# Kernel tuning notes

Hardware: AMD Instinct MI355X
Metric: run time of the kernel (lower is better)

Reference implementation:

```python
import jax, jax.numpy as jnp
import numpy as np
import math

B, S, E, A, H, L, V = 2, 2048, 512, 512, 8, 4, 50257
HD = A // H  # 64 per-head dim (attention_size // n_heads)
PAD = 0
EPS = 1e-5

def _sin_pe():
    pos = np.arange(S)[:, None].astype(np.float32)
    div = np.exp(np.arange(0, E, 2).astype(np.float32) * (-math.log(10000.0) / E))
    pe = np.zeros((S, E), dtype=np.float32)
    pe[:, 0::2] = np.sin(pos * div)
    pe[:, 1::2] = np.cos(pos * div)
    return jnp.asarray(pe)

PE = _sin_pe()

def setup_inputs():
    key = jax.random.key(0)
    ks = jax.random.split(key, 20)
    s = 0.02
    emb = jax.random.normal(ks[0], (V, E), jnp.float32) * s
    emb = emb.at[PAD].set(0.0)  # nn.Embedding padding_idx row is zero
    return {
        "input_ids": jax.random.randint(ks[1], (B, S), 0, V, dtype=jnp.int32),
        "attention_mask": jnp.ones((B, S), jnp.int32),
        "emb": emb,
        "Wq": jax.random.normal(ks[2], (L, H, E, HD), jnp.float32) * s,
        "Wk": jax.random.normal(ks[3], (L, H, E, HD), jnp.float32) * s,
        "Wv": jax.random.normal(ks[4], (L, H, E, HD), jnp.float32) * s,
        "Wo": jax.random.normal(ks[5], (L, A, E), jnp.float32) * s,
        "ln1_g": jnp.ones((L, E), jnp.float32),
        "ln1_b": jnp.zeros((L, E), jnp.float32),
        "ln2_g": jnp.ones((L, E), jnp.float32),
        "ln2_b": jnp.zeros((L, E), jnp.float32),
        "ff_w1": jax.random.normal(ks[6], (L, E, 4 * E), jnp.float32) * s,
        "ff_b1": jnp.zeros((L, 4 * E), jnp.float32),
        "ff_w2": jax.random.normal(ks[7], (L, 4 * E, E), jnp.float32) * s,
        "ff_b2": jnp.zeros((L, E), jnp.float32),
        "lnf_g": jnp.ones((E,), jnp.float32),
        "lnf_b": jnp.zeros((E,), jnp.float32),
        "Wout": jax.random.normal(ks[8], (E, V), jnp.float32) * s,
        "bout": jnp.zeros((V,), jnp.float32),
    }

def _ln(x, g, b):
    m = jnp.mean(x, axis=-1, keepdims=True)
    v = jnp.mean((x - m) ** 2, axis=-1, keepdims=True)
    return (x - m) / jnp.sqrt(v + EPS) * g + b

def reference(input_ids, attention_mask, emb, Wq, Wk, Wv, Wo, ln1_g, ln1_b, ln2_g, ln2_b, ff_w1, ff_b1, ff_w2, ff_b2, lnf_g, lnf_b, Wout, bout):
    # mask: padding (attention_mask==0) broadcast over queries, OR causal upper triangle
    pad = (attention_mask == 0)[:, None, :]                  # [B,1,S]
    causal = jnp.triu(jnp.ones((S, S), bool), 1)             # [S,S]
    mask = (pad | causal)[:, None, :, :]                     # [B,1,S,S]
    x = emb[input_ids] + PE[None, :S]                        # [B,S,E]
    scale = 1.0 / math.sqrt(HD)

    def block(x, p):
        wq, wk, wv, wo, g1, b1, g2, b2, w1, c1, w2, c2 = p
        xn = _ln(x, g1, b1)
        q = jnp.einsum('bse,hed->bhsd', xn, wq)
        k = jnp.einsum('bse,hed->bhsd', xn, wk)
        v = jnp.einsum('bse,hed->bhsd', xn, wv)
        scores = jnp.einsum('bhsd,bhtd->bhst', q, k) * scale  # masked_fill(-inf) then /sqrt(dk) == mask after scale
        scores = jnp.where(mask, -jnp.inf, scores)
        p_attn = jax.nn.softmax(scores, axis=-1)
        attn = jnp.einsum('bhst,bhtd->bhsd', p_attn, v)
        attn = attn.transpose(0, 2, 1, 3).reshape(B, S, A)    # concat heads
        x = x + attn @ wo                                     # residual + out proj (no bias)
        xn2 = _ln(x, g2, b2)
        h = jax.nn.gelu(xn2 @ w1 + c1, approximate=False)     # nn.GELU default (erf)
        x = x + h @ w2 + c2
        return x, None

    params = (Wq, Wk, Wv, Wo, ln1_g, ln1_b, ln2_g, ln2_b, ff_w1, ff_b1, ff_w2, ff_b2)
    x, _ = jax.lax.scan(block, x, params)
    return _ln(x, lnf_g, lnf_b) @ Wout + bout                 # [B,S,V]
```

## Files before the change

kernel.cpp:

```cpp
#include <hip/hip_runtime.h>
#include <math.h>

#define BB 2
#define SS 2048
#define EE 512
#define HH 8
#define HD 64
#define LL 4
#define VV 50257
#define NTOK (BB*SS)
#define VPAD2 50432

typedef __bf16 bf16_t;
typedef bf16_t bf16x8 __attribute__((ext_vector_type(8)));
typedef float  f32x4  __attribute__((ext_vector_type(4)));

__device__ __forceinline__ void gload_lds16(const void* g, void* l) {
  __builtin_amdgcn_global_load_lds(
      (const __attribute__((address_space(1))) void*)g,
      (__attribute__((address_space(3))) void*)l, 16, 0, 0);
}

__global__ __launch_bounds__(256) void embed_ln_kernel(
    const int* __restrict__ ids, const float* __restrict__ emb,
    const float* __restrict__ g, const float* __restrict__ b,
    float* __restrict__ x, bf16_t* __restrict__ xn) {
  int wv = threadIdx.x >> 6, lane = threadIdx.x & 63;
  int row = blockIdx.x * 4 + wv;
  int s = row & (SS - 1);
  int id = ids[row];
  const float* er = emb + (size_t)id * EE;
  float v[8];
  float sum = 0.f;
#pragma unroll
  for (int j = 0; j < 8; j++) {
    int e = lane * 8 + j;
    float freq = __expf((float)(e & ~1) * -0.01798894604f);
    float ang  = (float)s * freq;
    float pe   = (e & 1) ? __cosf(ang) : __sinf(ang);
    v[j] = er[e] + pe;
    sum += v[j];
  }
  float4* xp = reinterpret_cast<float4*>(x + (size_t)row * EE + lane * 8);
  xp[0] = make_float4(v[0], v[1], v[2], v[3]);
  xp[1] = make_float4(v[4], v[5], v[6], v[7]);
#pragma unroll
  for (int o = 32; o > 0; o >>= 1) sum += __shfl_xor(sum, o);
  float mean = sum * (1.f / EE);
  float var = 0.f;
#pragma unroll
  for (int j = 0; j < 8; j++) { float d = v[j] - mean; var += d * d; }
#pragma unroll
  for (int o = 32; o > 0; o >>= 1) var += __shfl_xor(var, o);
  float inv = rsqrtf(var * (1.f / EE) + 1e-5f);
  bf16_t tmp[8];
#pragma unroll
  for (int j = 0; j < 8; j++) {
    int e = lane * 8 + j;
    tmp[j] = (bf16_t)((v[j] - mean) * inv * g[e] + b[e]);
  }
  *reinterpret_cast<bf16x8*>(xn + (size_t)row * EE + lane * 8) = *reinterpret_cast<bf16x8*>(tmp);
}

__global__ __launch_bounds__(256) void ln_kernel(const float* __restrict__ in,
                                                 bf16_t* __restrict__ out,
                                                 const float* __restrict__ g,
                                                 const float* __restrict__ b) {
  int wv = threadIdx.x >> 6, lane = threadIdx.x & 63;
  int row = blockIdx.x * 4 + wv;
  const float4* r = reinterpret_cast<const float4*>(in + (size_t)row * EE) + lane * 2;
  float4 v0 = r[0], v1 = r[1];
  float s = v0.x + v0.y + v0.z + v0.w + v1.x + v1.y + v1.z + v1.w;
#pragma unroll
  for (int o = 32; o > 0; o >>= 1) s += __shfl_xor(s, o);
  float mean = s * (1.f / EE);
  float d0 = v0.x-mean, d1 = v0.y-mean, d2 = v0.z-mean, d3 = v0.w-mean;
  float d4 = v1.x-mean, d5 = v1.y-mean, d6 = v1.z-mean, d7 = v1.w-mean;
  float var = d0*d0+d1*d1+d2*d2+d3*d3+d4*d4+d5*d5+d6*d6+d7*d7;
#pragma unroll
  for (int o = 32; o > 0; o >>= 1) var += __shfl_xor(var, o);
  float inv = rsqrtf(var * (1.f / EE) + 1e-5f);
  const float4* gp = reinterpret_cast<const float4*>(g) + lane * 2;
  const float4* bp = reinterpret_cast<const float4*>(b) + lane * 2;
  float4 g0 = gp[0], g1 = gp[1], b0 = bp[0], b1 = bp[1];
  bf16_t tmp[8];
  tmp[0] = (bf16_t)(d0*inv*g0.x + b0.x); tmp[1] = (bf16_t)(d1*inv*g0.y + b0.y);
  tmp[2] = (bf16_t)(d2*inv*g0.z + b0.z); tmp[3] = (bf16_t)(d3*inv*g0.w + b0.w);
  tmp[4] = (bf16_t)(d4*inv*g1.x + b1.x); tmp[5] = (bf16_t)(d5*inv*g1.y + b1.y);
  tmp[6] = (bf16_t)(d6*inv*g1.z + b1.z); tmp[7] = (bf16_t)(d7*inv*g1.w + b1.w);
  *reinterpret_cast<bf16x8*>(out + (size_t)row * EE + lane * 8) = *reinterpret_cast<bf16x8*>(tmp);
}

__device__ __forceinline__ void transpose_tile(const float* __restrict__ ip,
                                               bf16_t* __restrict__ op,
                                               int k0, int n0, int ldin, int ldout,
                                               int Nvalid, float* T) {
  int t = threadIdx.x;
  int r = t >> 2, cb = (t & 3) * 16;
#pragma unroll
  for (int i = 0; i < 16; i++) {
    int n = n0 + cb + i;
    T[r * 65 + cb + i] = (n < Nvalid) ? ip[(size_t)(k0 + r) * ldin + n] : 0.f;
  }
  __syncthreads();
  bf16_t tmp[16];
#pragma unroll
  for (int i = 0; i < 16; i++) tmp[i] = (bf16_t)T[(cb + i) * 65 + r];
  bf16_t* o = op + (size_t)(n0 + r) * ldout + k0 + cb;
  *reinterpret_cast<bf16x8*>(o)     = *reinterpret_cast<bf16x8*>(&tmp[0]);
  *reinterpret_cast<bf16x8*>(o + 8) = *reinterpret_cast<bf16x8*>(&tmp[8]);
}

__global__ __launch_bounds__(256) void wconv_all(
    const float* __restrict__ Wq, const float* __restrict__ Wk,
    const float* __restrict__ Wv, const float* __restrict__ Wo,
    const float* __restrict__ fw1, const float* __restrict__ fw2,
    const float* __restrict__ Wout,
    bf16_t* Wqkv, bf16_t* WoT, bf16_t* W1T, bf16_t* W2T, bf16_t* WoutT) {
  __shared__ float T[64 * 65];
  int bid = blockIdx.x;
  if (bid < 768) {
    int kx = bid & 7, z = bid >> 3;
    int l = z / 24, rem = z % 24, sec = rem >> 3, h = rem & 7;
    const float* W = sec == 0 ? Wq : (sec == 1 ? Wk : Wv);
    const float* ip = W + (size_t)(l * 8 + h) * (EE * HD);
    bf16_t* op = Wqkv + (size_t)l * (1536 * 512) + (size_t)(sec * 512 + h * 64) * 512;
    transpose_tile(ip, op, kx * 64, 0, HD, EE, HD, T);
  } else if (bid < 1024) {
    int r = bid - 768;
    int kx = r & 7, ny = (r >> 3) & 7, l = r >> 6;
    transpose_tile(Wo + (size_t)l * 512 * 512, WoT + (size_t)l * 512 * 512,
                   kx * 64, ny * 64, 512, 512, 512, T);
  } else if (bid < 2048) {
    int r = bid - 1024;
    int kx = r & 7, ny = (r >> 3) & 31, l = r >> 8;
    transpose_tile(fw1 + (size_t)l * 512 * 2048, W1T + (size_t)l * 2048 * 512,
                   kx * 64, ny * 64, 2048, 512, 2048, T);
  } else if (bid < 3072) {
    int r = bid - 2048;
    int kx = r & 31, ny = (r >> 5) & 7, l = r >> 8;
    transpose_tile(fw2 + (size_t)l * 2048 * 512, W2T + (size_t)l * 512 * 2048,
                   kx * 64, ny * 64, 512, 2048, 512, T);
  } else {
    int r = bid - 3072;
    int kx = r & 7, ny = r >> 3;
    transpose_tile(Wout, WoutT, kx * 64, ny * 64, VV, 512, VV, T);
  }
}

template<int MODE>
__global__ __launch_bounds__(256) void gemm3_64(
    const bf16_t* __restrict__ A, const bf16_t* __restrict__ Bt,
    int M, int N, int K,
    const float* __restrict__ bias, bf16_t* __restrict__ Cb,
    bf16_t* __restrict__ qo, bf16_t* __restrict__ ko, bf16_t* __restrict__ vo) {
  constexpr int TM = 64, MI = 2;
  __shared__ __align__(16) bf16_t As[3][TM * 64];
  __shared__ __align__(16) bf16_t Bs[3][128 * 64];
  int tid = threadIdx.x, lane = tid & 63, w = tid >> 6;
  int lr = lane & 15, lg = lane >> 4;
  int m0 = blockIdx.y * TM, n0 = blockIdx.x * 128;
  f32x4 acc[MI][4];
#pragma unroll
  for (int i = 0; i < MI; i++)
#pragma unroll
    for (int j = 0; j < 4; j++) acc[i][j] = (f32x4){0.f, 0.f, 0.f, 0.f};
  int wr = w >> 1, wc = w & 1;

  const bf16_t* Abase = A  + (size_t)(m0 + lr) * K + lg * 8;
  const bf16_t* Bbase = Bt + (size_t)(n0 + lr) * K + lg * 8;

  auto stage = [&](int buf, int k0) {
#pragma unroll
    for (int i = 0; i < MI; i++) {
      int c = w * MI + i;
      gload_lds16(Abase + (size_t)(c >> 1) * 16 * K + k0 + (c & 1) * 32,
                  (char*)&As[buf][0] + c * 1024);
    }
#pragma unroll
    for (int i = 0; i < 4; i++) {
      int c = w * 4 + i;
      gload_lds16(Bbase + (size_t)(c >> 1) * 16 * K + k0 + (c & 1) * 32,
                  (char*)&Bs[buf][0] + c * 1024);
    }
  };

  int nk = K >> 6;
  stage(0, 0);
  if (nk > 1) stage(1, 64);
  for (int k = 0; k < nk; k++) {
    int cur = k % 3;
    if (k + 1 < nk) asm volatile("s_waitcnt vmcnt(6)" ::: "memory");
    else            asm volatile("s_waitcnt vmcnt(0)" ::: "memory");
    __builtin_amdgcn_s_barrier();
    __builtin_amdgcn_s_setprio(1);
#pragma unroll
    for (int kk = 0; kk < 2; kk++) {
      bf16x8 afr[MI], bfr[4];
#pragma unroll
      for (int mi = 0; mi < MI; mi++)
        afr[mi] = *reinterpret_cast<const bf16x8*>(
            &As[cur][(((wr * MI + mi) << 1) + kk) * 512 + lane * 8]);
#pragma unroll
      for (int ni = 0; ni < 4; ni++)
        bfr[ni] = *reinterpret_cast<const bf16x8*>(
            &Bs[cur][(((wc * 4 + ni) << 1) + kk) * 512 + lane * 8]);
#pragma unroll
      for (int mi = 0; mi < MI; mi++)
#pragma unroll
        for (int ni = 0; ni < 4; ni++)
          acc[mi][ni] = __builtin_amdgcn_mfma_f32_16x16x32_bf16(afr[mi], bfr[ni], acc[mi][ni], 0, 0, 0);
    }
    __builtin_amdgcn_s_setprio(0);
    if (k + 2 < nk) stage((k + 2) % 3, (k + 2) << 6);
  }

#pragma unroll
  for (int mi = 0; mi < MI; mi++)
#pragma unroll
    for (int ni = 0; ni < 4; ni++) {
      int colg = n0 + wc * 64 + ni * 16 + lr;
#pragma unroll
      for (int j = 0; j < 4; j++) {
        int rowg = m0 + wr * (TM / 2) + mi * 16 + lg * 4 + j;
        float v = acc[mi][ni][j];
        if (MODE == 0) {
          int sec = colg >> 9, cc = colg & 511, hh = cc >> 6, dd = cc & 63;
          int bi = rowg >> 11, s = rowg & 2047;
          if (sec == 0)      qo[(((size_t)bi * HH + hh) * SS + s) * HD + dd] = (bf16_t)(v * 0.125f);
          else if (sec == 1) ko[(((size_t)bi * HH + hh) * SS + s) * HD + dd] = (bf16_t)v;
          else               vo[(((size_t)bi * HH + hh) * HD + dd) * SS + s] = (bf16_t)v;
        } else {
          v += bias[colg];
          v = 0.5f * v * (1.f + erff(v * 0.70710678f));
          Cb[(size_t)rowg * N + colg] = (bf16_t)v;
        }
      }
    }
}

template<int MODE, int TM>
__global__ __launch_bounds__(256) void gemm_bf16(
    const bf16_t* __restrict__ A, const bf16_t* __restrict__ Bt,
    int M, int N, int K,
    const float* __restrict__ bias,
    float* __restrict__ Cf, bf16_t* __restrict__ Cb) {
  constexpr int MI = TM / 32;
  constexpr int LW = MI + 4;
  __shared__ __align__(16) bf16_t As[2][TM * 64];
  __shared__ __align__(16) bf16_t Bs[2][128 * 64];
  int tid = threadIdx.x, lane = tid & 63, w = tid >> 6;
  int lr = lane & 15, lg = lane >> 4;
  int m0 = blockIdx.y * TM, n0 = blockIdx.x * 128;
  f32x4 acc[MI][4];
#pragma unroll
  for (int i = 0; i < MI; i++)
#pragma unroll
    for (int j = 0; j < 4; j++) acc[i][j] = (f32x4){0.f, 0.f, 0.f, 0.f};
  int wr = w >> 1, wc = w & 1;

  const bf16_t* Abase = A  + (size_t)(m0 + lr) * K + lg * 8;
  const bf16_t* Bbase = Bt + (size_t)(n0 + lr) * K + lg * 8;

  auto stage = [&](int buf, int k0) {
#pragma unroll
    for (int i = 0; i < MI; i++) {
      int c = w * MI + i;
      gload_lds16(Abase + (size_t)(c >> 1) * 16 * K + k0 + (c & 1) * 32,
                  (char*)&As[buf][0] + c * 1024);
    }
#pragma unroll
    for (int i = 0; i < 4; i++) {
      int c = w * 4 + i;
      gload_lds16(Bbase + (size_t)(c >> 1) * 16 * K + k0 + (c & 1) * 32,
                  (char*)&Bs[buf][0] + c * 1024);
    }
  };

  int nk = K >> 6;
  stage(0, 0);
  for (int k = 0; k < nk; k++) {
    int cur = k & 1;
    if (k + 1 < nk) {
      stage(cur ^ 1, (k + 1) << 6);
      asm volatile("s_waitcnt vmcnt(%0)" :: "i"(LW) : "memory");
    } else {
      asm volatile("s_waitcnt vmcnt(0)" ::: "memory");
    }
    __builtin_amdgcn_s_barrier();
    __builtin_amdgcn_s_setprio(1);
#pragma unroll
    for (int kk = 0; kk < 2; kk++) {
      bf16x8 afr[MI], bfr[4];
#pragma unroll
      for (int mi = 0; mi < MI; mi++)
        afr[mi] = *reinterpret_cast<const bf16x8*>(
            &As[cur][(((wr * MI + mi) << 1) + kk) * 512 + lane * 8]);
#pragma unroll
      for (int ni = 0; ni < 4; ni++)
        bfr[ni] = *reinterpret_cast<const bf16x8*>(
            &Bs[cur][(((wc * 4 + ni) << 1) + kk) * 512 + lane * 8]);
#pragma unroll
      for (int mi = 0; mi < MI; mi++)
#pragma unroll
        for (int ni = 0; ni < 4; ni++)
          acc[mi][ni] = __builtin_amdgcn_mfma_f32_16x16x32_bf16(afr[mi], bfr[ni], acc[mi][ni], 0, 0, 0);
    }
    __builtin_amdgcn_s_setprio(0);
    __builtin_amdgcn_s_barrier();
  }

#pragma unroll
  for (int mi = 0; mi < MI; mi++)
#pragma unroll
    for (int ni = 0; ni < 4; ni++) {
      int colg = n0 + wc * 64 + ni * 16 + lr;
#pragma unroll
      for (int j = 0; j < 4; j++) {
        int rowg = m0 + wr * (TM / 2) + mi * 16 + lg * 4 + j;
        float v = acc[mi][ni][j];
        if (bias) v += bias[colg];
        Cf[(size_t)rowg * EE + colg] += v;
      }
    }
}

__global__ __launch_bounds__(512) void gemm256_out(
    const bf16_t* __restrict__ A, const bf16_t* __restrict__ Bt,
    const float* __restrict__ bias, float* __restrict__ C) {
  __shared__ __align__(16) char smem[64 * 260 * 4];
  bf16_t* As = (bf16_t*)smem;
  bf16_t* Bs = (bf16_t*)(smem + 32768);
  float*  Ep = (float*)smem;
  int tid = threadIdx.x, lane = tid & 63, w = tid >> 6;
  int lr = lane & 15, lg = lane >> 4;
  int bid = blockIdx.x;
  int n0 = (bid % 197) * 256, m0 = (bid / 197) * 256;
  int wr = w >> 2, wc = w & 3;
  f32x4 acc[8][4];
#pragma unroll
  for (int i = 0; i < 8; i++)
#pragma unroll
    for (int j = 0; j < 4; j++) acc[i][j] = (f32x4){0.f, 0.f, 0.f, 0.f};

  const bf16_t* Abase = A  + (size_t)(m0 + lr) * 512 + lg * 8;
  const bf16_t* Bbase = Bt + (size_t)(n0 + lr) * 512 + lg * 8;

  for (int k0 = 0; k0 < 512; k0 += 64) {
#pragma unroll
    for (int i = 0; i < 4; i++) {
      int c = w * 4 + i;
      gload_lds16(Abase + (size_t)(c >> 1) * 16 * 512 + k0 + (c & 1) * 32,
                  (char*)As + c * 1024);
      gload_lds16(Bbase + (size_t)(c >> 1) * 16 * 512 + k0 + (c & 1) * 32,
                  (char*)Bs + c * 1024);
    }
    __syncthreads();
#pragma unroll
    for (int kk = 0; kk < 2; kk++) {
      bf16x8 afr[8], bfr[4];
#pragma unroll
      for (int mi = 0; mi < 8; mi++)
        afr[mi] = *reinterpret_cast<const bf16x8*>(
            &As[(((wr * 8 + mi) << 1) + kk) * 512 + lane * 8]);
#pragma unroll
      for (int ni = 0; ni < 4; ni++)
        bfr[ni] = *reinterpret_cast<const bf16x8*>(
            &Bs[(((wc * 4 + ni) << 1) + kk) * 512 + lane * 8]);
#pragma unroll
      for (int mi = 0; mi < 8; mi++)
#pragma unroll
        for (int ni = 0; ni < 4; ni++)
          acc[mi][ni] = __builtin_amdgcn_mfma_f32_16x16x32_bf16(afr[mi], bfr[ni], acc[mi][ni], 0, 0, 0);
    }
    __syncthreads();
  }

  int colBase = n0 + (tid & 63) * 4;
  float b0 = 0.f, b1 = 0.f, b2 = 0.f, b3 = 0.f;
  if (colBase + 3 < VV) {
    float4 bv = *reinterpret_cast<const float4*>(bias + colBase);
    b0 = bv.x; b1 = bv.y; b2 = bv.z; b3 = bv.w;
  } else {
    if (colBase     < VV) b0 = bias[colBase];
    if (colBase + 1 < VV) b1 = bias[colBase + 1];
    if (colBase + 2 < VV) b2 = bias[colBase + 2];
  }
  int rw = tid >> 6;
  for (int ch = 0; ch < 4; ch++) {
    __syncthreads();
    if (wr == (ch >> 1)) {
      int mib = (ch & 1) * 4;
#pragma unroll
      for (int mi2 = 0; mi2 < 4; mi2++)
#pragma unroll
        for (int ni = 0; ni < 4; ni++) {
          int col = wc * 64 + ni * 16 + lr;
#pragma unroll
          for (int j = 0; j < 4; j++)
            Ep[(mi2 * 16 + lg * 4 + j) * 260 + col] = acc[mib + mi2][ni][j];
        }
    }
    __syncthreads();
#pragma unroll
    for (int pass = 0; pass < 8; pass++) {
      int r = pass * 8 + rw;
      f32x4 v = *reinterpret_cast<const f32x4*>(&Ep[r * 260 + (tid & 63) * 4]);
      v[0] += b0; v[1] += b1; v[2] += b2; v[3] += b3;
      float* dst = &C[(size_t)(m0 + ch * 64 + r) * VV + colBase];
      if (colBase + 3 < VV) {
        __builtin_nontemporal_store(v, reinterpret_cast<f32x4*>(dst));
      } else {
        if (colBase     < VV) __builtin_nontemporal_store(v[0], dst);
        if (colBase + 1 < VV) __builtin_nontemporal_store(v[1], dst + 1);
        if (colBase + 2 < VV) __builtin_nontemporal_store(v[2], dst + 2);
      }
    }
  }
}

#define QBLK 64
#define KVB 64
__global__ __launch_bounds__(256) void attn_kernel(
    const bf16_t* __restrict__ qb, const bf16_t* __restrict__ kb,
    const bf16_t* __restrict__ vT, const int* __restrict__ amask,
    bf16_t* __restrict__ ab) {
  __shared__ bf16_t Qs[QBLK][72];
  __shared__ bf16_t Ps[QBLK][72];
  __shared__ __align__(16) bf16_t Ks[3][KVB * 64];
  __shared__ __align__(16) bf16_t Vs[3][KVB * 64];
  __shared__ float kmAll[SS];
  int tid = threadIdx.x, lane = tid & 63, w = tid >> 6;
  int lr = lane & 15, lg = lane >> 4;
  int bid = blockIdx.x;
  int bh = bid & 15;
  int qi = bid >> 4;
  int qq = (qi < 16) ? qi : 47 - qi;
  int q0 = qq * QBLK;
  int b = bh >> 3, h = bh & 7;
  const bf16_t* Qg = qb + (size_t)bh * SS * HD;
  const bf16_t* Kg = kb + (size_t)bh * SS * HD;
  const bf16_t* Vg = vT + (size_t)bh * HD * SS;

  {
    int r = tid >> 2, c = (tid & 3) * 16;
    const uint4* s = reinterpret_cast<const uint4*>(Qg + (size_t)(q0 + r) * HD + c);
    uint4 a0 = s[0], a1 = s[1];
    *reinterpret_cast<uint4*>(&Qs[r][c])     = a0;
    *reinterpret_cast<uint4*>(&Qs[r][c + 8]) = a1;
  }
#pragma unroll
  for (int i = 0; i < 8; i++) {
    int s = i * 256 + tid;
    kmAll[s] = amask[b * SS + s] ? 0.f : -1e30f;
  }

  auto stageKV = [&](int buf, int kv0) {
#pragma unroll
    for (int i = 0; i < 4; i++) {
      int c = w * 4 + i;
      if (c < 8) {
        gload_lds16(Kg + (size_t)(kv0 + (c >> 1) * 16 + lr) * HD + (c & 1) * 32 + lg * 8,
                    (char*)&Ks[buf][0] + c * 1024);
      } else {
        int cc = c - 8;
        gload_lds16(Vg + (size_t)((cc >> 1) * 16 + lr) * SS + kv0 + (cc & 1) * 32 + lg * 8,
                    (char*)&Vs[buf][0] + cc * 1024);
      }
    }
  };

  f32x4 o[4];
  f32x4 m_run, l_run;
  m_run = (f32x4){-1e30f, -1e30f, -1e30f, -1e30f};
  l_run = (f32x4){0.f, 0.f, 0.f, 0.f};
#pragma unroll
  for (int nd = 0; nd < 4; nd++) o[nd] = (f32x4){0.f, 0.f, 0.f, 0.f};

  int ntile = qq + 1;
  stageKV(0, 0);
  if (ntile > 1) stageKV(1, KVB);
  __syncthreads();

  for (int t = 0; t < ntile; t++) {
    int buf = t % 3;
    int kv0 = t * KVB;
    if (t + 1 < ntile) asm volatile("s_waitcnt vmcnt(4)" ::: "memory");
    else               asm volatile("s_waitcnt vmcnt(0)" ::: "memory");
    __builtin_amdgcn_s_barrier();

    f32x4 sc[4];
#pragma unroll
    for (int ni = 0; ni < 4; ni++) sc[ni] = (f32x4){0.f, 0.f, 0.f, 0.f};
#pragma unroll
    for (int kk = 0; kk < 2; kk++) {
      bf16x8 af = *reinterpret_cast<const bf16x8*>(&Qs[w * 16 + lr][kk * 32 + lg * 8]);
      bf16x8 bf[4];
#pragma unroll
      for (int ni = 0; ni < 4; ni++)
        bf[ni] = *reinterpret_cast<const bf16x8*>(&Ks[buf][((ni << 1) + kk) * 512 + lane * 8]);
#pragma unroll
      for (int ni = 0; ni < 4; ni++)
        sc[ni] = __builtin_amdgcn_mfma_f32_16x16x32_bf16(af, bf[ni], sc[ni], 0, 0, 0);
    }

    {
      int qrb = q0 + w * 16 + lg * 4;
      float kmv[4];
#pragma unroll
      for (int ni = 0; ni < 4; ni++) kmv[ni] = kmAll[kv0 + ni * 16 + lr];
#pragma unroll
      for (int ni = 0; ni < 4; ni++) {
        int kg = kv0 + ni * 16 + lr;
#pragma unroll
        for (int j = 0; j < 4; j++) {
          float s = sc[ni][j] + kmv[ni];
          sc[ni][j] = (kg <= qrb + j) ? s : -1e30f;
        }
      }
      f32x4 rmax = sc[0];
#pragma unroll
      for (int ni = 1; ni < 4; ni++)
#pragma unroll
        for (int j = 0; j < 4; j++) rmax[j] = fmaxf(rmax[j], sc[ni][j]);
#pragma unroll
      for (int msk = 1; msk <= 8; msk <<= 1)
#pragma unroll
        for (int j = 0; j < 4; j++) rmax[j] = fmaxf(rmax[j], __shfl_xor(rmax[j], msk));
      f32x4 mnew, corr;
#pragma unroll
      for (int j = 0; j < 4; j++) {
        mnew[j] = fmaxf(m_run[j], rmax[j]);
        corr[j] = __expf(m_run[j] - mnew[j]);
      }
      m_run = mnew;
      f32x4 rs = (f32x4){0.f, 0.f, 0.f, 0.f};
#pragma unroll
      for (int ni = 0; ni < 4; ni++) {
#pragma unroll
        for (int j = 0; j < 4; j++) {
          float p = __expf(sc[ni][j] - mnew[j]);
          rs[j] += p;
          Ps[w * 16 + lg * 4 + j][ni * 16 + lr] = (bf16_t)p;
        }
      }
#pragma unroll
      for (int msk = 1; msk <= 8; msk <<= 1)
#pragma unroll
        for (int j = 0; j < 4; j++) rs[j] += __shfl_xor(rs[j], msk);
#pragma unroll
      for (int j = 0; j < 4; j++) l_run[j] = l_run[j] * corr[j] + rs[j];
#pragma unroll
      for (int nd = 0; nd < 4; nd++) o[nd] = o[nd] * corr;
    }

#pragma unroll
    for (int kc = 0; kc < 2; kc++) {
      bf16x8 pa = *reinterpret_cast<const bf16x8*>(&Ps[w * 16 + lr][kc * 32 + lg * 8]);
      bf16x8 vb[4];
#pragma unroll
      for (int nd = 0; nd < 4; nd++)
        vb[nd] = *reinterpret_cast<const bf16x8*>(&Vs[buf][((nd << 1) + kc) * 512 + lane * 8]);
#pragma unroll
      for (int nd = 0; nd < 4; nd++)
        o[nd] = __builtin_amdgcn_mfma_f32_16x16x32_bf16(pa, vb[nd], o[nd], 0, 0, 0);
    }

    if (t + 2 < ntile) stageKV((t + 2) % 3, kv0 + 2 * KVB);
  }

  f32x4 linv;
#pragma unroll
  for (int j = 0; j < 4; j++) linv[j] = 1.f / l_run[j];
#pragma unroll
  for (int nd = 0; nd < 4; nd++)
#pragma unroll
    for (int j = 0; j < 4; j++) {
      int rowg = b * SS + q0 + w * 16 + lg * 4 + j;
      int col = h * HD + nd * 16 + lr;
      ab[(size_t)rowg * EE + col] = (bf16_t)(o[nd][j] * linv[j]);
    }
}

extern "C" void kernel_launch(void* const* d_in, const int* in_sizes, int n_in,
                              void* d_out, int out_size, void* d_ws, size_t ws_size,
                              hipStream_t stream) {
  const int*   ids   = (const int*)d_in[0];
  const int*   amask = (const int*)d_in[1];
  const float* emb   = (const float*)d_in[2];
  const float* Wq    = (const float*)d_in[3];
  const float* Wk    = (const float*)d_in[4];
  const float* Wv    = (const float*)d_in[5];
  const float* Wo    = (const float*)d_in[6];
  const float* ln1g  = (const float*)d_in[7];
  const float* ln1b  = (const float*)d_in[8];
  const float* ln2g  = (const float*)d_in[9];
  const float* ln2b  = (const float*)d_in[10];
  const float* fw1   = (const float*)d_in[11];
  const float* fb1   = (const float*)d_in[12];
  const float* fw2   = (const float*)d_in[13];
  const float* fb2   = (const float*)d_in[14];
  const float* lnfg  = (const float*)d_in[15];
  const float* lnfb  = (const float*)d_in[16];
  const float* Wout  = (const float*)d_in[17];
  const float* bout  = (const float*)d_in[18];
  float* out = (float*)d_out;

  float*  x     = (float*)d_ws;
  bf16_t* xn    = (bf16_t*)((char*)d_ws + (8u << 20));
  bf16_t* WoutT = (bf16_t*)((char*)d_ws + (12u << 20));
  char* sc = (char*)d_out;
  bf16_t* qbuf = (bf16_t*)(sc);
  bf16_t* kbuf = (bf16_t*)(sc + 4194304);
  bf16_t* vTb  = (bf16_t*)(sc + 8388608);
  bf16_t* ab   = (bf16_t*)(sc + 12582912);
  bf16_t* hb   = (bf16_t*)(sc + 16777216);
  bf16_t* Wqkv = (bf16_t*)(sc + 33554432);
  bf16_t* WoT  = (bf16_t*)(sc + 39845888);
  bf16_t* W1T  = (bf16_t*)(sc + 41943040);
  bf16_t* W2T  = (bf16_t*)(sc + 50331648);

  wconv_all<<<dim3(3072 + 8 * (VPAD2 / 64)), 256, 0, stream>>>(
      Wq, Wk, Wv, Wo, fw1, fw2, Wout, Wqkv, WoT, W1T, W2T, WoutT);

  embed_ln_kernel<<<NTOK / 4, 256, 0, stream>>>(ids, emb, ln1g, ln1b, x, xn);

  for (int l = 0; l < LL; l++) {
    if (l > 0)
      ln_kernel<<<NTOK / 4, 256, 0, stream>>>(x, xn, ln1g + l * EE, ln1b + l * EE);
    gemm3_64<0><<<dim3(12, 64), 256, 0, stream>>>(xn, Wqkv + (size_t)l * 1536 * 512,
        NTOK, 1536, 512, nullptr, nullptr, qbuf, kbuf, vTb);
    attn_kernel<<<dim3(512), 256, 0, stream>>>(qbuf, kbuf, vTb, amask, ab);
    gemm_bf16<2, 32><<<dim3(4, 128), 256, 0, stream>>>(ab, WoT + (size_t)l * 512 * 512,
        NTOK, 512, 512, nullptr, x, nullptr);
    ln_kernel<<<NTOK / 4, 256, 0, stream>>>(x, xn, ln2g + l * EE, ln2b + l * EE);
    gemm3_64<1><<<dim3(16, 64), 256, 0, stream>>>(xn, W1T + (size_t)l * 2048 * 512,
        NTOK, 2048, 512, fb1 + l * 2048, hb, nullptr, nullptr, nullptr);
    gemm_bf16<2, 32><<<dim3(4, 128), 256, 0, stream>>>(hb, W2T + (size_t)l * 512 * 2048,
        NTOK, 512, 2048, fb2 + l * EE, x, nullptr);
  }
  ln_kernel<<<NTOK / 4, 256, 0, stream>>>(x, xn, lnfg, lnfb);
  gemm256_out<<<dim3(16 * (VPAD2 / 256)), 512, 0, stream>>>(xn, WoutT, bout, out);
}
```

Measured before the change: 1.279 ms.

## Fuse residual-add GEMMs with following LayerNorm via full-row tiles

Replaces the Wo and FFN2 residual GEMMs plus the separate LayerNorm kernels with one kernel that computes a 16-row by full-512-column tile per block, adds bias and the residual, then computes the row LayerNorm in-block and writes both x and bf16 xn. This removes the standalone LN launches and their extra read of x. In exchange, each block is tiny in M (16 rows), so the whole B matrix is reloaded per block with no double buffering. Variance is computed as E[x^2]-mean^2 in one pass, which is less numerically stable.

```diff
diff --git a/kernel.cpp b/kernel.cpp
--- a/kernel.cpp
+++ b/kernel.cpp
@@ -60,35 +60,6 @@
     tmp[j] = (bf16_t)((v[j] - mean) * inv * g[e] + b[e]);
   }
   *reinterpret_cast<bf16x8*>(xn + (size_t)row * EE + lane * 8) = *reinterpret_cast<bf16x8*>(tmp);
-}
-
-__global__ __launch_bounds__(256) void ln_kernel(const float* __restrict__ in,
-                                                 bf16_t* __restrict__ out,
-                                                 const float* __restrict__ g,
-                                                 const float* __restrict__ b) {
-  int wv = threadIdx.x >> 6, lane = threadIdx.x & 63;
-  int row = blockIdx.x * 4 + wv;
-  const float4* r = reinterpret_cast<const float4*>(in + (size_t)row * EE) + lane * 2;
-  float4 v0 = r[0], v1 = r[1];
-  float s = v0.x + v0.y + v0.z + v0.w + v1.x + v1.y + v1.z + v1.w;
-#pragma unroll
-  for (int o = 32; o > 0; o >>= 1) s += __shfl_xor(s, o);
-  float mean = s * (1.f / EE);
-  float d0 = v0.x-mean, d1 = v0.y-mean, d2 = v0.z-mean, d3 = v0.w-mean;
-  float d4 = v1.x-mean, d5 = v1.y-mean, d6 = v1.z-mean, d7 = v1.w-mean;
-  float var = d0*d0+d1*d1+d2*d2+d3*d3+d4*d4+d5*d5+d6*d6+d7*d7;
-#pragma unroll
-  for (int o = 32; o > 0; o >>= 1) var += __shfl_xor(var, o);
-  float inv = rsqrtf(var * (1.f / EE) + 1e-5f);
-  const float4* gp = reinterpret_cast<const float4*>(g) + lane * 2;
-  const float4* bp = reinterpret_cast<const float4*>(b) + lane * 2;
-  float4 g0 = gp[0], g1 = gp[1], b0 = bp[0], b1 = bp[1];
-  bf16_t tmp[8];
-  tmp[0] = (bf16_t)(d0*inv*g0.x + b0.x); tmp[1] = (bf16_t)(d1*inv*g0.y + b0.y);
-  tmp[2] = (bf16_t)(d2*inv*g0.z + b0.z); tmp[3] = (bf16_t)(d3*inv*g0.w + b0.w);
-  tmp[4] = (bf16_t)(d4*inv*g1.x + b1.x); tmp[5] = (bf16_t)(d5*inv*g1.y + b1.y);
-  tmp[6] = (bf16_t)(d6*inv*g1.z + b1.z); tmp[7] = (bf16_t)(d7*inv*g1.w + b1.w);
-  *reinterpret_cast<bf16x8*>(out + (size_t)row * EE + lane * 8) = *reinterpret_cast<bf16x8*>(tmp);
 }
 
 __device__ __forceinline__ void transpose_tile(const float* __restrict__ ip,
@@ -239,90 +210,111 @@
     }
 }
 
-template<int MODE, int TM>
-__global__ __launch_bounds__(256) void gemm_bf16(
-    const bf16_t* __restrict__ A, const bf16_t* __restrict__ Bt,
-    int M, int N, int K,
-    const float* __restrict__ bias,
-    float* __restrict__ Cf, bf16_t* __restrict__ Cb) {
-  constexpr int MI = TM / 32;
-  constexpr int LW = MI + 4;
-  __shared__ __align__(16) bf16_t As[2][TM * 64];
-  __shared__ __align__(16) bf16_t Bs[2][128 * 64];
+template<bool HASBIAS>
+__global__ __launch_bounds__(512) void gemm_ln(
+    const bf16_t* __restrict__ A, const bf16_t* __restrict__ Bt, int K,
+    const float* __restrict__ bias, float* x,
+    const float* __restrict__ g, const float* __restrict__ b,
+    bf16_t* __restrict__ xn) {
+  __shared__ __align__(16) bf16_t As[2 * 512];
+  __shared__ __align__(16) bf16_t Bs[64 * 512];
+  __shared__ float pSum[128], pSqr[128];
   int tid = threadIdx.x, lane = tid & 63, w = tid >> 6;
   int lr = lane & 15, lg = lane >> 4;
-  int m0 = blockIdx.y * TM, n0 = blockIdx.x * 128;
-  f32x4 acc[MI][4];
-#pragma unroll
-  for (int i = 0; i < MI; i++)
-#pragma unroll
-    for (int j = 0; j < 4; j++) acc[i][j] = (f32x4){0.f, 0.f, 0.f, 0.f};
-  int wr = w >> 1, wc = w & 1;
+  int m0 = blockIdx.x * 16;
+
+  f32x4 acc[4];
+#pragma unroll
+  for (int i = 0; i < 4; i++) acc[i] = (f32x4){0.f, 0.f, 0.f, 0.f};
 
   const bf16_t* Abase = A  + (size_t)(m0 + lr) * K + lg * 8;
-  const bf16_t* Bbase = Bt + (size_t)(n0 + lr) * K + lg * 8;
-
-  auto stage = [&](int buf, int k0) {
-#pragma unroll
-    for (int i = 0; i < MI; i++) {
-      int c = w * MI + i;
-      gload_lds16(Abase + (size_t)(c >> 1) * 16 * K + k0 + (c & 1) * 32,
-                  (char*)&As[buf][0] + c * 1024);
-    }
-#pragma unroll
-    for (int i = 0; i < 4; i++) {
-      int c = w * 4 + i;
-      gload_lds16(Bbase + (size_t)(c >> 1) * 16 * K + k0 + (c & 1) * 32,
-                  (char*)&Bs[buf][0] + c * 1024);
-    }
-  };
+  const bf16_t* Bbase = Bt + (size_t)lr * K + lg * 8;
 
   int nk = K >> 6;
-  stage(0, 0);
   for (int k = 0; k < nk; k++) {
-    int cur = k & 1;
-    if (k + 1 < nk) {
-      stage(cur ^ 1, (k + 1) << 6);
-      asm volatile("s_waitcnt vmcnt(%0)" :: "i"(LW) : "memory");
-    } else {
-      asm volatile("s_waitcnt vmcnt(0)" ::: "memory");
-    }
-    __builtin_amdgcn_s_barrier();
+    int k0 = k << 6;
+#pragma unroll
+    for (int i = 0; i < 8; i++) {
+      int cb = w * 8 + i;
+      gload_lds16(Bbase + (size_t)(cb >> 1) * 16 * K + k0 + (cb & 1) * 32,
+                  (char*)Bs + cb * 1024);
+    }
+    if (w < 2)
+      gload_lds16(Abase + k0 + w * 32, (char*)As + w * 1024);
+    __syncthreads();
     __builtin_amdgcn_s_setprio(1);
 #pragma unroll
     for (int kk = 0; kk < 2; kk++) {
-      bf16x8 afr[MI], bfr[4];
-#pragma unroll
-      for (int mi = 0; mi < MI; mi++)
-        afr[mi] = *reinterpret_cast<const bf16x8*>(
-            &As[cur][(((wr * MI + mi) << 1) + kk) * 512 + lane * 8]);
+      bf16x8 afr = *reinterpret_cast<const bf16x8*>(&As[kk * 512 + lane * 8]);
+      bf16x8 bfr[4];
 #pragma unroll
       for (int ni = 0; ni < 4; ni++)
         bfr[ni] = *reinterpret_cast<const bf16x8*>(
-            &Bs[cur][(((wc * 4 + ni) << 1) + kk) * 512 + lane * 8]);
-#pragma unroll
-      for (int mi = 0; mi < MI; mi++)
-#pragma unroll
-        for (int ni = 0; ni < 4; ni++)
-          acc[mi][ni] = __builtin_amdgcn_mfma_f32_16x16x32_bf16(afr[mi], bfr[ni], acc[mi][ni], 0, 0, 0);
+            &Bs[(((w * 4 + ni) << 1) + kk) * 512 + lane * 8]);
+#pragma unroll
+      for (int ni = 0; ni < 4; ni++)
+        acc[ni] = __builtin_amdgcn_mfma_f32_16x16x32_bf16(afr, bfr[ni], acc[ni], 0, 0, 0);
     }
     __builtin_amdgcn_s_setprio(0);
-    __builtin_amdgcn_s_barrier();
-  }
-
-#pragma unroll
-  for (int mi = 0; mi < MI; mi++)
-#pragma unroll
-    for (int ni = 0; ni < 4; ni++) {
-      int colg = n0 + wc * 64 + ni * 16 + lr;
-#pragma unroll
-      for (int j = 0; j < 4; j++) {
-        int rowg = m0 + wr * (TM / 2) + mi * 16 + lg * 4 + j;
-        float v = acc[mi][ni][j];
-        if (bias) v += bias[colg];
-        Cf[(size_t)rowg * EE + colg] += v;
-      }
-    }
+    __syncthreads();
+  }
+
+  float v[4][4];
+  float bi4[4];
+#pragma unroll
+  for (int ni = 0; ni < 4; ni++) {
+    int colg = w * 64 + ni * 16 + lr;
+    bi4[ni] = HASBIAS ? bias[colg] : 0.f;
+#pragma unroll
+    for (int j = 0; j < 4; j++) {
+      int rowg = m0 + lg * 4 + j;
+      v[ni][j] = acc[ni][j] + bi4[ni] + x[(size_t)rowg * EE + colg];
+    }
+  }
+  float s1[4], s2[4];
+#pragma unroll
+  for (int j = 0; j < 4; j++) { s1[j] = 0.f; s2[j] = 0.f; }
+#pragma unroll
+  for (int ni = 0; ni < 4; ni++)
+#pragma unroll
+    for (int j = 0; j < 4; j++) { s1[j] += v[ni][j]; s2[j] += v[ni][j] * v[ni][j]; }
+#pragma unroll
+  for (int msk = 1; msk <= 8; msk <<= 1)
+#pragma unroll
+    for (int j = 0; j < 4; j++) {
+      s1[j] += __shfl_xor(s1[j], msk);
+      s2[j] += __shfl_xor(s2[j], msk);
+    }
+  if (lr == 0) {
+#pragma unroll
+    for (int j = 0; j < 4; j++) {
+      pSum[w * 16 + lg * 4 + j] = s1[j];
+      pSqr[w * 16 + lg * 4 + j] = s2[j];
+    }
+  }
+  __syncthreads();
+  float mean[4], inv[4];
+#pragma unroll
+  for (int j = 0; j < 4; j++) {
+    int row = lg * 4 + j;
+    float t1 = 0.f, t2 = 0.f;
+#pragma unroll
+    for (int w2 = 0; w2 < 8; w2++) { t1 += pSum[w2 * 16 + row]; t2 += pSqr[w2 * 16 + row]; }
+    mean[j] = t1 * (1.f / EE);
+    float var = t2 * (1.f / EE) - mean[j] * mean[j];
+    inv[j] = rsqrtf(var + 1e-5f);
+  }
+#pragma unroll
+  for (int ni = 0; ni < 4; ni++) {
+    int colg = w * 64 + ni * 16 + lr;
+    float gg = g[colg], bb = b[colg];
+#pragma unroll
+    for (int j = 0; j < 4; j++) {
+      int rowg = m0 + lg * 4 + j;
+      x[(size_t)rowg * EE + colg] = v[ni][j];
+      xn[(size_t)rowg * EE + colg] = (bf16_t)((v[ni][j] - mean[j]) * inv[j] * gg + bb);
+    }
+  }
 }
 
 __global__ __launch_bounds__(512) void gemm256_out(
@@ -626,19 +618,18 @@
   embed_ln_kernel<<<NTOK / 4, 256, 0, stream>>>(ids, emb, ln1g, ln1b, x, xn);
 
   for (int l = 0; l < LL; l++) {
-    if (l > 0)
-      ln_kernel<<<NTOK / 4, 256, 0, stream>>>(x, xn, ln1g + l * EE, ln1b + l * EE);
     gemm3_64<0><<<dim3(12, 64), 256, 0, stream>>>(xn, Wqkv + (size_t)l * 1536 * 512,
         NTOK, 1536, 512, nullptr, nullptr, qbuf, kbuf, vTb);
     attn_kernel<<<dim3(512), 256, 0, stream>>>(qbuf, kbuf, vTb, amask, ab);
-    gemm_bf16<2, 32><<<dim3(4, 128), 256, 0, stream>>>(ab, WoT + (size_t)l * 512 * 512,
-        NTOK, 512, 512, nullptr, x, nullptr);
-    ln_kernel<<<NTOK / 4, 256, 0, stream>>>(x, xn, ln2g + l * EE, ln2b + l * EE);
+    gemm_ln<false><<<dim3(NTOK / 16), 512, 0, stream>>>(
+        ab, WoT + (size_t)l * 512 * 512, 512, nullptr, x,
+        ln2g + l * EE, ln2b + l * EE, xn);
     gemm3_64<1><<<dim3(16, 64), 256, 0, stream>>>(xn, W1T + (size_t)l * 2048 * 512,
         NTOK, 2048, 512, fb1 + l * 2048, hb, nullptr, nullptr, nullptr);
-    gemm_bf16<2, 32><<<dim3(4, 128), 256, 0, stream>>>(hb, W2T + (size_t)l * 512 * 2048,
-        NTOK, 512, 2048, fb2 + l * EE, x, nullptr);
-  }
-  ln_kernel<<<NTOK / 4, 256, 0, stream>>>(x, xn, lnfg, lnfb);
+    const float* gg = (l == LL - 1) ? lnfg : ln1g + (l + 1) * EE;
+    const float* bb = (l == LL - 1) ? lnfb : ln1b + (l + 1) * EE;
+    gemm_ln<true><<<dim3(NTOK / 16), 512, 0, stream>>>(
+        hb, W2T + (size_t)l * 512 * 2048, 2048, fb2 + l * EE, x, gg, bb, xn);
+  }
   gemm256_out<<<dim3(16 * (VPAD2 / 256)), 512, 0, stream>>>(xn, WoutT, bout, out);
 }
```

New measurement: 1.449 ms. 1.13x slower.
